# Performance work log

Measured on AMD Instinct MI355X. Metric: run time of the kernel, lower is better.

The kernel has to match this reference:

```python
import jax, jax.numpy as jnp
import numpy as np

K = 1024        # n_embeddings
D = 256         # embedding_dim
BETA = 0.25
EPS = 1e-10


def setup_inputs() -> dict:
    key = jax.random.key(0)
    k1, k2 = jax.random.split(key)
    inputs = jax.random.normal(k1, (64, D, 32, 32), dtype=jnp.float32)
    # codebook init matches nn.Embedding.weight.data.uniform_(-1/K, 1/K)
    embedding = jax.random.uniform(k2, (K, D), dtype=jnp.float32,
                                   minval=-1.0 / K, maxval=1.0 / K)
    return {"inputs": inputs, "embedding": embedding}


def reference(inputs, embedding):
    B, C, H, W = inputs.shape  # C == D
    # NCHW -> NHWC -> (N, D)
    z = jnp.transpose(inputs, (0, 2, 3, 1)).reshape(-1, C)
    N = z.shape[0]

    # squared distances ||z - e||^2 = ||z||^2 + ||e||^2 - 2 z.e  (GEMM-dominant)
    d = (jnp.sum(z * z, axis=1, keepdims=True)
         + jnp.sum(embedding * embedding, axis=1)[None, :]
         - 2.0 * (z @ embedding.T))                     # (N, K)
    idx = jnp.argmin(d, axis=1)                          # (N,) int

    z_q = embedding[idx]                                 # gather (N, D)

    # codebook + commitment loss
    loss = (jnp.mean((jax.lax.stop_gradient(z_q) - z) ** 2)
            + BETA * jnp.mean((z_q - jax.lax.stop_gradient(z)) ** 2))

    # straight-through estimator
    z_q_st = z + jax.lax.stop_gradient(z_q - z)

    # perplexity over codebook usage
    counts = jnp.zeros((K,), dtype=z.dtype).at[idx].add(1.0)
    probs = counts / N
    perplexity = jnp.exp(-jnp.sum(probs * jnp.log(probs + EPS)))

    z_q_out = jnp.transpose(z_q_st.reshape(B, H, W, C), (0, 3, 1, 2))
    return loss, z_q_out, perplexity
```

## Files before the change

### kernel.cpp

```cpp
#include <hip/hip_runtime.h>

#define D_   256
#define HW_  1024
#define N_   65536
#define K_   1024
#define ND_  16777216
#define MARGIN_A 2.0e-6f
#define MARGIN_B 3.5e-5f

typedef __attribute__((ext_vector_type(8))) short bf16x8;
typedef __attribute__((ext_vector_type(8))) _Float16 f16x8;
typedef __attribute__((ext_vector_type(4))) float f32x4;

union f16cv { _Float16 h; unsigned short u; };

__device__ inline unsigned short f16_bits(float v) {
    f16cv c; c.h = (_Float16)v; return c.u;
}

#define GLL16(g, l) __builtin_amdgcn_global_load_lds( \
    (const __attribute__((address_space(1))) unsigned int*)(const void*)(g), \
    (__attribute__((address_space(3))) unsigned int*)(void*)(l), 16, 0, 0)

__global__ __launch_bounds__(256) void k_init(const float* __restrict__ E,
                                              unsigned short* __restrict__ Eh,
                                              float* __restrict__ Et,
                                              float* __restrict__ e2f,
                                              double* __restrict__ e2d,
                                              int* __restrict__ counts,
                                              int* __restrict__ nflag_f,
                                              int* __restrict__ nflag_c,
                                              double* __restrict__ loss_acc) {
    __shared__ double sh[256];
    int k = blockIdx.x, t = threadIdx.x;
    float v = E[(size_t)k * D_ + t];
    Eh[(size_t)k * D_ + t] = f16_bits(v * 1024.f);
    Et[(size_t)t * K_ + k] = v;
    sh[t] = (double)v * v;
    __syncthreads();
    for (int off = 128; off; off >>= 1) {
        if (t < off) sh[t] += sh[t + off];
        __syncthreads();
    }
    if (t == 0) {
        e2f[k] = (float)sh[0];
        e2d[k] = sh[0];
        counts[k] = 0;
        if (k == 0) { *loss_acc = 0.0; *nflag_f = 0; *nflag_c = 0; }
    }
}

__global__ __launch_bounds__(256) void k_zsplit(const float* __restrict__ Z,
                                                unsigned short* __restrict__ Zh,
                                                float* __restrict__ S1) {
    __shared__ unsigned short lh[32][264];
    __shared__ float sabs[32][8];
    int t = threadIdx.x;
    int bid = blockIdx.x;
    int b = bid >> 5, hw0 = (bid & 31) * 32;
    int hw = t & 31, dq = t >> 5;
    const float* zb = Z + (size_t)b * (D_ * HW_) + hw0;
    float asum = 0.f;
    #pragma unroll 8
    for (int j = 0; j < 32; ++j) {
        int d = j * 8 + dq;
        float v = zb[(size_t)d * HW_ + hw];
        lh[hw][d] = f16_bits(v);
        asum += fabsf(v);
    }
    sabs[hw][dq] = asum;
    __syncthreads();
    int row = t >> 3, cb = t & 7;
    size_t nbase = ((size_t)b * HW_ + hw0 + row) * D_;
    #pragma unroll
    for (int jj = 0; jj < 4; ++jj) {
        int ch = cb + jj * 8;
        *(bf16x8*)(Zh + nbase + ch * 8) = *(const bf16x8*)&lh[row][ch * 8];
    }
    if (t < 32) {
        float s = 0.f;
        #pragma unroll
        for (int q = 0; q < 8; ++q) s += sabs[t][q];
        S1[(size_t)b * HW_ + hw0 + t] = s;
    }
}

__global__ __launch_bounds__(256) void k_phase1(const unsigned short* __restrict__ Zh,
                                                const unsigned short* __restrict__ Eh,
                                                const float* __restrict__ e2f,
                                                float* __restrict__ pm1,
                                                float* __restrict__ pm2,
                                                int* __restrict__ pi1) {
    __shared__ __align__(16) unsigned short lds[4 * 8192];
    int t = threadIdx.x, w = t >> 6, l = t & 63;
    int bid = blockIdx.x;
    int xcd = bid & 7, slot = bid >> 3;
    int mb = xcd * 64 + (slot >> 3);
    int nb = slot & 7;
    int wr = w >> 1, wc = w & 1;

    const unsigned short* src =
        (w < 2 ? Zh + (size_t)mb * 128 * D_ : Eh + (size_t)nb * 128 * D_)
        + (size_t)(w & 1) * 64 * D_;
    unsigned short* myl0 = &lds[__builtin_amdgcn_readfirstlane(w * 4096)];
    unsigned short* myl1 = &lds[__builtin_amdgcn_readfirstlane(16384 + w * 4096)];

    int Rl = l >> 3;
    int lc = (l & 7) ^ (l >> 3);

    f32x4 acc[4][4];
    #pragma unroll
    for (int m = 0; m < 4; ++m)
        #pragma unroll
        for (int nn = 0; nn < 4; ++nn) acc[m][nn] = (f32x4){0.f, 0.f, 0.f, 0.f};

    for (int ktp = 0; ktp < 2; ++ktp) {
        #pragma unroll
        for (int i = 0; i < 8; ++i) {
            const unsigned short* g = src + (size_t)(i * 8 + Rl) * D_ + (ktp * 2) * 64 + lc * 8;
            GLL16(g, myl0 + i * 512);
        }
        #pragma unroll
        for (int i = 0; i < 8; ++i) {
            const unsigned short* g = src + (size_t)(i * 8 + Rl) * D_ + (ktp * 2 + 1) * 64 + lc * 8;
            GLL16(g, myl1 + i * 512);
        }
        __syncthreads();
        int q = l >> 4;
        #pragma unroll
        for (int kt2 = 0; kt2 < 2; ++kt2) {
            const char* Ab = (const char*)lds + kt2 * 32768;
            const char* Bb = Ab + 16384;
            #pragma unroll
            for (int ks2 = 0; ks2 < 2; ++ks2) {
                int pcb = ((ks2 * 4 + q) ^ (l & 7)) * 16;
                f16x8 ah[4];
                #pragma unroll
                for (int m = 0; m < 4; ++m)
                    ah[m] = *(const f16x8*)(Ab + (wr * 64 + m * 16 + (l & 15)) * 128 + pcb);
                #pragma unroll
                for (int nn = 0; nn < 4; ++nn) {
                    f16x8 bh = *(const f16x8*)(Bb + (wc * 64 + nn * 16 + (l & 15)) * 128 + pcb);
                    #pragma unroll
                    for (int m = 0; m < 4; ++m)
                        acc[m][nn] = __builtin_amdgcn_mfma_f32_16x16x32_f16(ah[m], bh, acc[m][nn], 0, 0, 0);
                }
            }
        }
        __syncthreads();
    }

    float m1v[4][4], m2v[4][4]; int i1v[4][4];
    #pragma unroll
    for (int m = 0; m < 4; ++m)
        #pragma unroll
        for (int r = 0; r < 4; ++r) { m1v[m][r] = 3.4e38f; m2v[m][r] = 3.4e38f; i1v[m][r] = 0; }

    #pragma unroll
    for (int nn = 0; nn < 4; ++nn) {
        int c = nb * 128 + wc * 64 + nn * 16 + (l & 15);
        float e2 = e2f[c];
        #pragma unroll
        for (int m = 0; m < 4; ++m)
            #pragma unroll
            for (int r = 0; r < 4; ++r) {
                float s = fmaf(-2.f / 1024.f, acc[m][nn][r], e2);
                if (s < m1v[m][r])      { m2v[m][r] = m1v[m][r]; m1v[m][r] = s; i1v[m][r] = c; }
                else if (s < m2v[m][r]) { m2v[m][r] = s; }
            }
    }
    #pragma unroll
    for (int off = 1; off < 16; off <<= 1) {
        #pragma unroll
        for (int m = 0; m < 4; ++m)
            #pragma unroll
            for (int r = 0; r < 4; ++r) {
                float o1 = __shfl_xor(m1v[m][r], off, 64);
                float o2 = __shfl_xor(m2v[m][r], off, 64);
                int   oi = __shfl_xor(i1v[m][r], off, 64);
                if (o1 < m1v[m][r]) { m2v[m][r] = fminf(m1v[m][r], o2); m1v[m][r] = o1; i1v[m][r] = oi; }
                else                { m2v[m][r] = fminf(m2v[m][r], o1); }
            }
    }
    __syncthreads();
    float* ex1 = (float*)lds;
    float* ex2 = ex1 + 256;
    int*   exi = (int*)(ex2 + 256);
    if ((l & 15) == 0) {
        int qq = l >> 4;
        #pragma unroll
        for (int m = 0; m < 4; ++m)
            #pragma unroll
            for (int r = 0; r < 4; ++r) {
                int e = (wr * 2 + wc) * 64 + m * 16 + qq * 4 + r;
                ex1[e] = m1v[m][r]; ex2[e] = m2v[m][r]; exi[e] = i1v[m][r];
            }
    }
    __syncthreads();
    if (t < 128) {
        int wr2 = t >> 6, rw = t & 63;
        int e0 = (wr2 * 2 + 0) * 64 + rw, e1 = (wr2 * 2 + 1) * 64 + rw;
        float a1 = ex1[e0], a2 = ex2[e0]; int ai = exi[e0];
        float b1 = ex1[e1], b2 = ex2[e1]; int bi = exi[e1];
        float M1, M2; int I1;
        if (a1 <= b1) { M1 = a1; I1 = ai; M2 = fminf(a2, b1); }
        else          { M1 = b1; I1 = bi; M2 = fminf(b2, a1); }
        size_t p = (size_t)nb * N_ + (size_t)mb * 128 + t;
        pm1[p] = M1; pm2[p] = M2; pi1[p] = I1;
    }
}

__global__ __launch_bounds__(256) void k_merge(const float* __restrict__ pm1,
                                               const float* __restrict__ pm2,
                                               const int* __restrict__ pi1,
                                               const float* __restrict__ S1,
                                               int* __restrict__ idx,
                                               int* __restrict__ counts,
                                               int* __restrict__ c8,
                                               unsigned char* __restrict__ ncand,
                                               int* __restrict__ list_c,
                                               int* __restrict__ nflag_c,
                                               int* __restrict__ list_f,
                                               int* __restrict__ nflag_f) {
    int n = blockIdx.x * 256 + threadIdx.x;
    float a1[8], a2[8]; int ai[8];
    float M1 = 3.4e38f, M2 = 3.4e38f; int I1 = 0;
    #pragma unroll
    for (int nb = 0; nb < 8; ++nb) {
        size_t p = (size_t)nb * N_ + n;
        a1[nb] = pm1[p]; a2[nb] = pm2[p]; ai[nb] = pi1[p];
        if (a1[nb] < M1) { M2 = fminf(M1, a2[nb]); M1 = a1[nb]; I1 = ai[nb]; }
        else             { M2 = fminf(M2, a1[nb]); }
    }
    idx[n] = I1;
    atomicAdd(&counts[I1], 1);
    float thr = M1 + fmaf(S1[n], MARGIN_A, MARGIN_B);
    bool fl = M2 < thr;
    bool needfull = false;
    int cnt = 0;
    if (fl) {
        #pragma unroll
        for (int nb = 0; nb < 8; ++nb) {
            if (a2[nb] < thr) needfull = true;
            if (a1[nb] < thr) ++cnt;
        }
    }
    bool candrow = fl && !needfull;
    bool fullrow = fl && needfull;
    if (candrow) {
        ncand[n] = (unsigned char)cnt;
        int pos = 0;
        #pragma unroll
        for (int nb = 0; nb < 8; ++nb)
            if (a1[nb] < thr) c8[(size_t)n * 8 + (pos++)] = ai[nb];
    }
    int lane = threadIdx.x & 63;
    unsigned long long mc = __ballot(candrow);
    if (mc) {
        int base = 0;
        if (lane == 0) base = atomicAdd(nflag_c, __popcll(mc));
        base = __shfl(base, 0, 64);
        if (candrow) list_c[base + __popcll(mc & ((1ull << lane) - 1ull))] = n;
    }
    unsigned long long mf = __ballot(fullrow);
    if (mf) {
        int base = 0;
        if (lane == 0) base = atomicAdd(nflag_f, __popcll(mf));
        base = __shfl(base, 0, 64);
        if (fullrow) list_f[base + __popcll(mf & ((1ull << lane) - 1ull))] = n;
    }
}

__global__ __launch_bounds__(256) void k_cand2(const float* __restrict__ Z,
                                               const float* __restrict__ E,
                                               const double* __restrict__ e2d,
                                               const int* __restrict__ c8,
                                               const unsigned char* __restrict__ ncand,
                                               const int* __restrict__ list_c,
                                               const int* __restrict__ nflag_c,
                                               int* __restrict__ idx,
                                               int* __restrict__ counts) {
    int t = threadIdx.x, w = t >> 6, l = t & 63;
    int nf = *nflag_c;
    int gw = blockIdx.x * 4 + w;
    for (int ii = gw; ii < nf; ii += 1024) {
        int n = list_c[ii];
        int b = n >> 10, hw = n & (HW_ - 1);
        const float* zp = Z + (size_t)b * (D_ * HW_) + hw;
        double z0 = (double)zp[(size_t)(l      ) * HW_];
        double z1 = (double)zp[(size_t)(l +  64) * HW_];
        double z2 = (double)zp[(size_t)(l + 128) * HW_];
        double z3 = (double)zp[(size_t)(l + 192) * HW_];
        int nc = ncand[n];
        double bv = 1e300; int bi = 0;
        for (int j = 0; j < nc; ++j) {
            int c = c8[(size_t)n * 8 + j];
            const float* er = E + (size_t)c * D_;
            double s = z0 * (double)er[l];
            s = fma(z1, (double)er[l +  64], s);
            s = fma(z2, (double)er[l + 128], s);
            s = fma(z3, (double)er[l + 192], s);
            #pragma unroll
            for (int off = 32; off; off >>= 1) s += __shfl_xor(s, off, 64);
            double sc = fma(-2.0, s, e2d[c]);
            if (sc < bv || (sc == bv && c < bi)) { bv = sc; bi = c; }
        }
        if (l == 0) {
            int old = idx[n];
            if (bi != old) {
                idx[n] = bi;
                atomicSub(&counts[old], 1);
                atomicAdd(&counts[bi], 1);
            }
        }
    }
}

__global__ __launch_bounds__(256) void k_rescan8(const float* __restrict__ Z,
                                                 const float* __restrict__ Et,
                                                 const double* __restrict__ e2d,
                                                 const int* __restrict__ list_f,
                                                 const int* __restrict__ nflag_f,
                                                 int* __restrict__ idx,
                                                 int* __restrict__ counts) {
    __shared__ float  zs[8][257];
    __shared__ int    sn[8];
    __shared__ double rbv[8][4];
    __shared__ int    rbi[8][4];
    int t = threadIdx.x, w = t >> 6, l = t & 63;
    int nf = *nflag_f;

    double ed0 = e2d[4 * t + 0], ed1 = e2d[4 * t + 1];
    double ed2 = e2d[4 * t + 2], ed3 = e2d[4 * t + 3];

    for (int ch = blockIdx.x; ch * 8 < nf; ch += gridDim.x) {
        __syncthreads();
        int i0 = ch * 8;
        int vc = min(8, nf - i0);
        if (t < 8) sn[t] = list_f[i0 + min(t, vc - 1)];
        __syncthreads();

        #pragma unroll
        for (int j = 0; j < 8; ++j) {
            int n = sn[j];
            zs[j][t] = Z[(size_t)(n >> 10) * (D_ * HW_) + (size_t)t * HW_ + (n & (HW_ - 1))];
        }
        __syncthreads();

        double s[8][4];
        #pragma unroll
        for (int r = 0; r < 8; ++r)
            s[r][0] = s[r][1] = s[r][2] = s[r][3] = 0.0;

        for (int d0 = 0; d0 < 256; d0 += 8) {
            float4 e4v[8];
            #pragma unroll
            for (int u = 0; u < 8; ++u)
                e4v[u] = *(const float4*)(Et + (size_t)(d0 + u) * K_ + 4 * t);
            #pragma unroll
            for (int u = 0; u < 8; ++u) {
                double ex = (double)e4v[u].x, ey = (double)e4v[u].y;
                double ez = (double)e4v[u].z, ew = (double)e4v[u].w;
                #pragma unroll
                for (int r = 0; r < 8; ++r) {
                    double zv = (double)zs[r][d0 + u];
                    s[r][0] = fma(zv, ex, s[r][0]);
                    s[r][1] = fma(zv, ey, s[r][1]);
                    s[r][2] = fma(zv, ez, s[r][2]);
                    s[r][3] = fma(zv, ew, s[r][3]);
                }
            }
        }

        #pragma unroll
        for (int r = 0; r < 8; ++r) {
            double bv = fma(-2.0, s[r][0], ed0); int bi = 4 * t;
            double c1 = fma(-2.0, s[r][1], ed1);
            double c2 = fma(-2.0, s[r][2], ed2);
            double c3 = fma(-2.0, s[r][3], ed3);
            if (c1 < bv) { bv = c1; bi = 4 * t + 1; }
            if (c2 < bv) { bv = c2; bi = 4 * t + 2; }
            if (c3 < bv) { bv = c3; bi = 4 * t + 3; }
            #pragma unroll
            for (int off = 1; off < 64; off <<= 1) {
                double ov = __shfl_xor(bv, off, 64);
                int    oi = __shfl_xor(bi, off, 64);
                if (ov < bv || (ov == bv && oi < bi)) { bv = ov; bi = oi; }
            }
            if (l == 0) { rbv[r][w] = bv; rbi[r][w] = bi; }
        }
        __syncthreads();

        if (t < vc) {
            double bv = rbv[t][0]; int bi = rbi[t][0];
            #pragma unroll
            for (int ww = 1; ww < 4; ++ww) {
                double ov = rbv[t][ww]; int oi = rbi[t][ww];
                if (ov < bv || (ov == bv && oi < bi)) { bv = ov; bi = oi; }
            }
            int n = sn[t];
            int old = idx[n];
            if (bi != old) {
                idx[n] = bi;
                atomicSub(&counts[old], 1);
                atomicAdd(&counts[bi], 1);
            }
        }
    }
}

__global__ __launch_bounds__(256) void k_gather(const float* __restrict__ Z,
                                                const float* __restrict__ E,
                                                const int* __restrict__ idx,
                                                float* __restrict__ out_zq,
                                                double* __restrict__ loss_acc) {
    __shared__ float ecache[32][257];
    __shared__ int sidx[32];
    __shared__ double wls[4];
    int t = threadIdx.x;
    int n0 = blockIdx.x * 32;
    int b = n0 >> 10, hw0 = n0 & (HW_ - 1);
    if (t < 32) sidx[t] = idx[n0 + t];
    __syncthreads();
    #pragma unroll 8
    for (int j = 0; j < 32; ++j)
        ecache[j][t] = E[(size_t)sidx[j] * D_ + t];
    __syncthreads();
    int hw = t & 31, cq = t >> 5;
    const float* zb = Z      + (size_t)b * (D_ * HW_) + hw0 + hw;
    float*       ob = out_zq + (size_t)b * (D_ * HW_) + hw0 + hw;
    double ls = 0.0;
    #pragma unroll 4
    for (int jj = 0; jj < 32; ++jj) {
        int c = cq * 32 + jj;
        float e = ecache[hw][c];
        float z = zb[(size_t)c * HW_];
        ob[(size_t)c * HW_] = e;
        double dz = (double)z - (double)e;
        ls = fma(dz, dz, ls);
    }
    #pragma unroll
    for (int off = 32; off; off >>= 1) ls += __shfl_xor(ls, off, 64);
    int wv = t >> 6;
    if ((t & 63) == 0) wls[wv] = ls;
    __syncthreads();
    if (t == 0) atomicAdd(loss_acc, wls[0] + wls[1] + wls[2] + wls[3]);
}

__global__ __launch_bounds__(256) void k_final(const int* __restrict__ counts,
                                               const double* __restrict__ loss_acc,
                                               float* __restrict__ out) {
    __shared__ double sh[256];
    int t = threadIdx.x;
    double s = 0.0;
    for (int k = t; k < K_; k += 256) {
        double p = (double)counts[k] / (double)N_;
        s += p * log(p + 1e-10);
    }
    sh[t] = s; __syncthreads();
    for (int off = 128; off; off >>= 1) {
        if (t < off) sh[t] += sh[t + off];
        __syncthreads();
    }
    if (t == 0) {
        out[0]       = (float)((*loss_acc) / (double)ND_ * 1.25);
        out[1 + ND_] = (float)exp(-sh[0]);
    }
}

extern "C" void kernel_launch(void* const* d_in, const int* in_sizes, int n_in,
                              void* d_out, int out_size, void* d_ws, size_t ws_size,
                              hipStream_t stream) {
    (void)in_sizes; (void)n_in; (void)out_size; (void)ws_size;
    const float* Z = (const float*)d_in[0];
    const float* E = (const float*)d_in[1];
    float* out = (float*)d_out;

    char* ws = (char*)d_ws;
    unsigned short* Zh       = (unsigned short*)(ws);
    unsigned short* Eh       = (unsigned short*)(ws + 33554432);
    float*          Et       = (float*)(ws + 34078720);
    float*          e2f      = (float*)(ws + 35127296);
    double*         e2d      = (double*)(ws + 35131392);
    float*          S1       = (float*)(ws + 35139584);
    float*          pm1      = (float*)(ws + 35401728);
    float*          pm2      = (float*)(ws + 37498880);
    int*            pi1      = (int*)  (ws + 39596032);
    int*            idx      = (int*)  (ws + 41693184);
    int*            list_f   = (int*)  (ws + 42020864);
    int*            list_c   = (int*)  (ws + 42283008);
    int*            c8       = (int*)  (ws + 42545152);
    unsigned char*  ncand    = (unsigned char*)(ws + 44642304);
    int*            counts   = (int*)  (ws + 44707840);
    int*            nflag_f  = (int*)  (ws + 44711936);
    int*            nflag_c  = (int*)  (ws + 44712000);
    double*         loss_acc = (double*)(ws + 44712064);

    k_init   <<<dim3(1024), dim3(256), 0, stream>>>(E, Eh, Et, e2f, e2d, counts, nflag_f, nflag_c, loss_acc);
    k_zsplit <<<dim3(2048), dim3(256), 0, stream>>>(Z, Zh, S1);
    k_phase1 <<<dim3(4096), dim3(256), 0, stream>>>(Zh, Eh, e2f, pm1, pm2, pi1);
    k_merge  <<<dim3(256),  dim3(256), 0, stream>>>(pm1, pm2, pi1, S1, idx, counts,
                                                    c8, ncand, list_c, nflag_c, list_f, nflag_f);
    k_cand2  <<<dim3(256),  dim3(256), 0, stream>>>(Z, E, e2d, c8, ncand, list_c, nflag_c, idx, counts);
    k_rescan8<<<dim3(1024), dim3(256), 0, stream>>>(Z, Et, e2d, list_f, nflag_f, idx, counts);
    k_gather <<<dim3(2048), dim3(256), 0, stream>>>(Z, E, idx, out + 1, loss_acc);
    k_final  <<<1,          dim3(256), 0, stream>>>(counts, loss_acc, out);
}
```

Before: 252.2 us.

## Compute loss algebraically from distances and fuse candidate and rescan fixup kernels

```diff
diff --git a/kernel.cpp b/kernel.cpp
--- a/kernel.cpp
+++ b/kernel.cpp
@@ -52,24 +52,35 @@
 
 __global__ __launch_bounds__(256) void k_zsplit(const float* __restrict__ Z,
                                                 unsigned short* __restrict__ Zh,
-                                                float* __restrict__ S1) {
+                                                float* __restrict__ S1,
+                                                double* __restrict__ loss_acc) {
     __shared__ unsigned short lh[32][264];
     __shared__ float sabs[32][8];
+    __shared__ double dsh[256];
     int t = threadIdx.x;
     int bid = blockIdx.x;
     int b = bid >> 5, hw0 = (bid & 31) * 32;
     int hw = t & 31, dq = t >> 5;
     const float* zb = Z + (size_t)b * (D_ * HW_) + hw0;
     float asum = 0.f;
+    double qsum = 0.0;
     #pragma unroll 8
     for (int j = 0; j < 32; ++j) {
         int d = j * 8 + dq;
         float v = zb[(size_t)d * HW_ + hw];
         lh[hw][d] = f16_bits(v);
         asum += fabsf(v);
+        qsum = fma((double)v, (double)v, qsum);
     }
     sabs[hw][dq] = asum;
-    __syncthreads();
+    dsh[t] = qsum;
+    __syncthreads();
+    for (int off = 128; off; off >>= 1) {
+        if (t < off) dsh[t] += dsh[t + off];
+        __syncthreads();
+    }
+    if (t == 0) atomicAdd(loss_acc, dsh[0]);
+
     int row = t >> 3, cb = t & 7;
     size_t nbase = ((size_t)b * HW_ + hw0 + row) * D_;
     #pragma unroll
@@ -221,7 +232,9 @@
                                                int* __restrict__ list_c,
                                                int* __restrict__ nflag_c,
                                                int* __restrict__ list_f,
-                                               int* __restrict__ nflag_f) {
+                                               int* __restrict__ nflag_f,
+                                               double* __restrict__ loss_acc) {
+    __shared__ double msh[256];
     int n = blockIdx.x * 256 + threadIdx.x;
     float a1[8], a2[8]; int ai[8];
     float M1 = 3.4e38f, M2 = 3.4e38f; int I1 = 0;
@@ -269,71 +282,75 @@
         base = __shfl(base, 0, 64);
         if (fullrow) list_f[base + __popcll(mf & ((1ull << lane) - 1ull))] = n;
     }
-}
-
-__global__ __launch_bounds__(256) void k_cand2(const float* __restrict__ Z,
+    msh[threadIdx.x] = (double)M1;
+    __syncthreads();
+    for (int off = 128; off; off >>= 1) {
+        if (threadIdx.x < off) msh[threadIdx.x] += msh[threadIdx.x + off];
+        __syncthreads();
+    }
+    if (threadIdx.x == 0) atomicAdd(loss_acc, msh[0]);
+}
+
+__global__ __launch_bounds__(256) void k_fixup(const float* __restrict__ Z,
                                                const float* __restrict__ E,
+                                               const float* __restrict__ Et,
                                                const double* __restrict__ e2d,
                                                const int* __restrict__ c8,
                                                const unsigned char* __restrict__ ncand,
                                                const int* __restrict__ list_c,
                                                const int* __restrict__ nflag_c,
+                                               const int* __restrict__ list_f,
+                                               const int* __restrict__ nflag_f,
                                                int* __restrict__ idx,
                                                int* __restrict__ counts) {
-    int t = threadIdx.x, w = t >> 6, l = t & 63;
-    int nf = *nflag_c;
-    int gw = blockIdx.x * 4 + w;
-    for (int ii = gw; ii < nf; ii += 1024) {
-        int n = list_c[ii];
-        int b = n >> 10, hw = n & (HW_ - 1);
-        const float* zp = Z + (size_t)b * (D_ * HW_) + hw;
-        double z0 = (double)zp[(size_t)(l      ) * HW_];
-        double z1 = (double)zp[(size_t)(l +  64) * HW_];
-        double z2 = (double)zp[(size_t)(l + 128) * HW_];
-        double z3 = (double)zp[(size_t)(l + 192) * HW_];
-        int nc = ncand[n];
-        double bv = 1e300; int bi = 0;
-        for (int j = 0; j < nc; ++j) {
-            int c = c8[(size_t)n * 8 + j];
-            const float* er = E + (size_t)c * D_;
-            double s = z0 * (double)er[l];
-            s = fma(z1, (double)er[l +  64], s);
-            s = fma(z2, (double)er[l + 128], s);
-            s = fma(z3, (double)er[l + 192], s);
-            #pragma unroll
-            for (int off = 32; off; off >>= 1) s += __shfl_xor(s, off, 64);
-            double sc = fma(-2.0, s, e2d[c]);
-            if (sc < bv || (sc == bv && c < bi)) { bv = sc; bi = c; }
-        }
-        if (l == 0) {
-            int old = idx[n];
-            if (bi != old) {
-                idx[n] = bi;
-                atomicSub(&counts[old], 1);
-                atomicAdd(&counts[bi], 1);
-            }
-        }
-    }
-}
-
-__global__ __launch_bounds__(256) void k_rescan8(const float* __restrict__ Z,
-                                                 const float* __restrict__ Et,
-                                                 const double* __restrict__ e2d,
-                                                 const int* __restrict__ list_f,
-                                                 const int* __restrict__ nflag_f,
-                                                 int* __restrict__ idx,
-                                                 int* __restrict__ counts) {
     __shared__ float  zs[8][257];
     __shared__ int    sn[8];
     __shared__ double rbv[8][4];
     __shared__ int    rbi[8][4];
     int t = threadIdx.x, w = t >> 6, l = t & 63;
+
+    if (blockIdx.x >= 1024) {
+        int nf = *nflag_c;
+        int gw = (blockIdx.x - 1024) * 4 + w;
+        for (int ii = gw; ii < nf; ii += 1024) {
+            int n = list_c[ii];
+            int b = n >> 10, hw = n & (HW_ - 1);
+            const float* zp = Z + (size_t)b * (D_ * HW_) + hw;
+            double z0 = (double)zp[(size_t)(l      ) * HW_];
+            double z1 = (double)zp[(size_t)(l +  64) * HW_];
+            double z2 = (double)zp[(size_t)(l + 128) * HW_];
+            double z3 = (double)zp[(size_t)(l + 192) * HW_];
+            int nc = ncand[n];
+            double bv = 1e300; int bi = 0;
+            for (int j = 0; j < nc; ++j) {
+                int c = c8[(size_t)n * 8 + j];
+                const float* er = E + (size_t)c * D_;
+                double s = z0 * (double)er[l];
+                s = fma(z1, (double)er[l +  64], s);
+                s = fma(z2, (double)er[l + 128], s);
+                s = fma(z3, (double)er[l + 192], s);
+                #pragma unroll
+                for (int off = 32; off; off >>= 1) s += __shfl_xor(s, off, 64);
+                double sc = fma(-2.0, s, e2d[c]);
+                if (sc < bv || (sc == bv && c < bi)) { bv = sc; bi = c; }
+            }
+            if (l == 0) {
+                int old = idx[n];
+                if (bi != old) {
+                    idx[n] = bi;
+                    atomicSub(&counts[old], 1);
+                    atomicAdd(&counts[bi], 1);
+                }
+            }
+        }
+        return;
+    }
+
     int nf = *nflag_f;
-
     double ed0 = e2d[4 * t + 0], ed1 = e2d[4 * t + 1];
     double ed2 = e2d[4 * t + 2], ed3 = e2d[4 * t + 3];
 
-    for (int ch = blockIdx.x; ch * 8 < nf; ch += gridDim.x) {
+    for (int ch = blockIdx.x; ch * 8 < nf; ch += 1024) {
         __syncthreads();
         int i0 = ch * 8;
         int vc = min(8, nf - i0);
@@ -409,14 +426,11 @@
     }
 }
 
-__global__ __launch_bounds__(256) void k_gather(const float* __restrict__ Z,
-                                                const float* __restrict__ E,
+__global__ __launch_bounds__(256) void k_gather(const float* __restrict__ E,
                                                 const int* __restrict__ idx,
-                                                float* __restrict__ out_zq,
-                                                double* __restrict__ loss_acc) {
+                                                float* __restrict__ out_zq) {
     __shared__ float ecache[32][257];
     __shared__ int sidx[32];
-    __shared__ double wls[4];
     int t = threadIdx.x;
     int n0 = blockIdx.x * 32;
     int b = n0 >> 10, hw0 = n0 & (HW_ - 1);
@@ -427,24 +441,12 @@
         ecache[j][t] = E[(size_t)sidx[j] * D_ + t];
     __syncthreads();
     int hw = t & 31, cq = t >> 5;
-    const float* zb = Z      + (size_t)b * (D_ * HW_) + hw0 + hw;
-    float*       ob = out_zq + (size_t)b * (D_ * HW_) + hw0 + hw;
-    double ls = 0.0;
-    #pragma unroll 4
+    float* ob = out_zq + (size_t)b * (D_ * HW_) + hw0 + hw;
+    #pragma unroll 8
     for (int jj = 0; jj < 32; ++jj) {
         int c = cq * 32 + jj;
-        float e = ecache[hw][c];
-        float z = zb[(size_t)c * HW_];
-        ob[(size_t)c * HW_] = e;
-        double dz = (double)z - (double)e;
-        ls = fma(dz, dz, ls);
-    }
-    #pragma unroll
-    for (int off = 32; off; off >>= 1) ls += __shfl_xor(ls, off, 64);
-    int wv = t >> 6;
-    if ((t & 63) == 0) wls[wv] = ls;
-    __syncthreads();
-    if (t == 0) atomicAdd(loss_acc, wls[0] + wls[1] + wls[2] + wls[3]);
+        ob[(size_t)c * HW_] = ecache[hw][c];
+    }
 }
 
 __global__ __launch_bounds__(256) void k_final(const int* __restrict__ counts,
@@ -497,12 +499,12 @@
     double*         loss_acc = (double*)(ws + 44712064);
 
     k_init   <<<dim3(1024), dim3(256), 0, stream>>>(E, Eh, Et, e2f, e2d, counts, nflag_f, nflag_c, loss_acc);
-    k_zsplit <<<dim3(2048), dim3(256), 0, stream>>>(Z, Zh, S1);
+    k_zsplit <<<dim3(2048), dim3(256), 0, stream>>>(Z, Zh, S1, loss_acc);
     k_phase1 <<<dim3(4096), dim3(256), 0, stream>>>(Zh, Eh, e2f, pm1, pm2, pi1);
     k_merge  <<<dim3(256),  dim3(256), 0, stream>>>(pm1, pm2, pi1, S1, idx, counts,
-                                                    c8, ncand, list_c, nflag_c, list_f, nflag_f);
-    k_cand2  <<<dim3(256),  dim3(256), 0, stream>>>(Z, E, e2d, c8, ncand, list_c, nflag_c, idx, counts);
-    k_rescan8<<<dim3(1024), dim3(256), 0, stream>>>(Z, Et, e2d, list_f, nflag_f, idx, counts);
-    k_gather <<<dim3(2048), dim3(256), 0, stream>>>(Z, E, idx, out + 1, loss_acc);
+                                                    c8, ncand, list_c, nflag_c, list_f, nflag_f, loss_acc);
+    k_fixup  <<<dim3(1280), dim3(256), 0, stream>>>(Z, E, Et, e2d, c8, ncand,
+                                                    list_c, nflag_c, list_f, nflag_f, idx, counts);
+    k_gather <<<dim3(2048), dim3(256), 0, stream>>>(E, idx, out + 1);
     k_final  <<<1,          dim3(256), 0, stream>>>(counts, loss_acc, out);
 }
```

Result: faster. 240.4 us (-4.7%).
